# Kernel tuning notes

Hardware: AMD Instinct MI355X
Metric: run time of the kernel (lower is better)

Reference implementation:

```python
import jax, jax.numpy as jnp
import numpy as np

S, B, D = 128, 32, 512
H = 512
L = 2
V = 8000


def _mk_lstm_params(key, in_dim, hid, layers):
    ks = jax.random.split(key, 4 * layers)
    s = 1.0 / np.sqrt(hid)
    W_ih = jnp.stack([jax.random.uniform(ks[4 * j + 0], (4 * hid, in_dim if j == 0 else hid), minval=-s, maxval=s) for j in range(layers)])
    W_hh = jnp.stack([jax.random.uniform(ks[4 * j + 1], (4 * hid, hid), minval=-s, maxval=s) for j in range(layers)])
    b_ih = jnp.stack([jax.random.uniform(ks[4 * j + 2], (4 * hid,), minval=-s, maxval=s) for j in range(layers)])
    b_hh = jnp.stack([jax.random.uniform(ks[4 * j + 3], (4 * hid,), minval=-s, maxval=s) for j in range(layers)])
    return W_ih, W_hh, b_ih, b_hh


def setup_inputs() -> dict:
    key = jax.random.key(0)
    kx, kf, kb, kwf, kwb = jax.random.split(key, 5)
    x = jax.random.normal(kx, (S, B, D), dtype=jnp.float32)
    Wf_ih, Wf_hh, bf_ih, bf_hh = _mk_lstm_params(kf, D, H, L)
    Wb_ih, Wb_hh, bb_ih, bb_hh = _mk_lstm_params(kb, D, H, L)
    s = 1.0 / np.sqrt(H)
    W_fwd = jax.random.uniform(kwf, (V, H), minval=-s, maxval=s)
    b_fwd = jnp.zeros((V,), jnp.float32)
    W_bwd = jax.random.uniform(kwb, (V, H), minval=-s, maxval=s)
    b_bwd = jnp.zeros((V,), jnp.float32)
    return {"x": x,
            "Wf_ih": Wf_ih, "Wf_hh": Wf_hh, "bf_ih": bf_ih, "bf_hh": bf_hh,
            "Wb_ih": Wb_ih, "Wb_hh": Wb_hh, "bb_ih": bb_ih, "bb_hh": bb_hh,
            "W_fwd": W_fwd, "b_fwd": b_fwd, "W_bwd": W_bwd, "b_bwd": b_bwd}


def _stacked_lstm(x_seq, W_ih, W_hh, b_ih, b_hh):
    """x_seq: [S,B,D]; params stacked over layers [L,4H,*]. Returns top-layer h over time: [S,B,H]."""
    layers = W_ih.shape[0]
    batch = x_seq.shape[1]
    h0 = jnp.zeros((layers, batch, H), x_seq.dtype)
    c0 = jnp.zeros((layers, batch, H), x_seq.dtype)

    def step(carry, x_t):
        h, c = carry
        hs, cs = [], []
        inp = x_t
        for j in range(layers):
            gates = inp @ W_ih[j].T + b_ih[j] + h[j] @ W_hh[j].T + b_hh[j]  # [B,4H]
            i_g, f_g, g_g, o_g = jnp.split(gates, 4, axis=-1)
            c_j = jax.nn.sigmoid(f_g) * c[j] + jax.nn.sigmoid(i_g) * jnp.tanh(g_g)
            h_j = jax.nn.sigmoid(o_g) * jnp.tanh(c_j)
            hs.append(h_j)
            cs.append(c_j)
            inp = h_j
        return (jnp.stack(hs), jnp.stack(cs)), inp

    _, out = jax.lax.scan(step, (h0, c0), x_seq)
    return out  # [S,B,H]


def reference(x, Wf_ih, Wf_hh, bf_ih, bf_hh, Wb_ih, Wb_hh, bb_ih, bb_hh, W_fwd, b_fwd, W_bwd, b_bwd):
    fwd_h = _stacked_lstm(x, Wf_ih, Wf_hh, bf_ih, bf_hh)                    # [S,B,H]
    bwd_h = _stacked_lstm(x[::-1], Wb_ih, Wb_hh, bb_ih, bb_hh)[::-1]        # [S,B,H]
    forward_dis = fwd_h @ W_fwd.T + b_fwd                                   # [S,B,V]
    backward_dis = bwd_h @ W_bwd.T + b_bwd                                  # [S,B,V]
    return (forward_dis, backward_dis)
```

## Files before the change

kernel.cpp:

```cpp
#include <hip/hip_runtime.h>

#define SS 128
#define BB 32
#define HH 512
#define VV 8000
#define VPAD 8064

typedef __bf16 bf16_t;
typedef __bf16 bf16x8 __attribute__((ext_vector_type(8)));
typedef float  floatx4 __attribute__((ext_vector_type(4)));
typedef unsigned int u32x4 __attribute__((ext_vector_type(4)));

__device__ __forceinline__ float sigmoidf_(float x) { return 1.0f / (1.0f + expf(-x)); }
__device__ __forceinline__ bf16x8 as_bf16x8(u32x4 v) { return __builtin_bit_cast(bf16x8, v); }

#define WS_FLG   0
#define WS_HHI   1024
#define WS_HLO   (WS_HHI + 524288)
#define WS_XHI   (WS_HLO + 524288)
#define WS_XLO   (WS_XHI + 4194304)
#define WS_HOUT  (WS_XLO + 4194304)
#define WS_WP    (WS_HOUT + 8388608)
#define MEMSET_BYTES WS_XHI

#define SMEM_BYTES 149632


__global__ __launch_bounds__(256)
void prep_x(const float* __restrict__ x, bf16_t* __restrict__ xh, bf16_t* __restrict__ xl) {
    int i = blockIdx.x * 256 + threadIdx.x;
    float v = x[i];
    bf16_t h = (bf16_t)v;
    xh[i] = h;
    xl[i] = (bf16_t)(v - (float)h);
}

__global__ __launch_bounds__(256)
void prep_wp(const float* __restrict__ Wf, const float* __restrict__ Wb, bf16_t* __restrict__ Wp) {
    int i = blockIdx.x * 256 + threadIdx.x;
    int k   = i & 511;
    int rd  = i >> 9;
    int row = rd % 8064;
    int d   = rd / 8064;
    const float* W = d ? Wb : Wf;
    Wp[i] = (row < VV) ? (bf16_t)W[(size_t)row * 512 + k] : (bf16_t)0.0f;
}


__global__ __launch_bounds__(512, 2)
void lstm_persist(const float* __restrict__ Wf_ih, const float* __restrict__ Wf_hh,
                  const float* __restrict__ Wb_ih, const float* __restrict__ Wb_hh,
                  const float* __restrict__ bf_ih, const float* __restrict__ bf_hh,
                  const float* __restrict__ bb_ih, const float* __restrict__ bb_hh,
                  const bf16_t* __restrict__ x_hi, const bf16_t* __restrict__ x_lo,
                  bf16_t* __restrict__ h_hi, bf16_t* __restrict__ h_lo,
                  bf16_t* __restrict__ hout, int* __restrict__ flg)
{
    extern __shared__ char smem[];
    bf16_t* wlds = (bf16_t*)smem;
    float*  pbuf = (float*)(smem + 131072);
    float*  bsum = (float*)(smem + 131072 + 18432);

    const int bid  = blockIdx.x;
    const int d    = bid >> 7;
    const int l    = (bid >> 6) & 1;
    const int s    = bid & 63;
    const int gid  = d * 2 + l;
    const int tid  = threadIdx.x;
    const int lane = tid & 63;
    const int kq   = tid >> 6;
    const int half = kq >> 2;
    const int kb   = kq & 3;
    const int lrow = lane & 15;
    const int quad = lane >> 4;

    const float* Wih = (d ? Wb_ih : Wf_ih) + (size_t)l * (2048 * 512);
    const float* Whh = (d ? Wb_hh : Wf_hh) + (size_t)l * (2048 * 512);

    if (tid < 32) {
        int g = tid >> 3, c = tid & 7;
        int grow = g * 512 + s * 8 + c;
        bsum[tid] = (d ? bb_ih : bf_ih)[l * 2048 + grow] + (d ? bb_hh : bf_hh)[l * 2048 + grow];
    }

    {
        const float* Wsrc = half ? Whh : Wih;
        bf16x8* w8 = (bf16x8*)wlds;
#pragma unroll
        for (int j = 0; j < 4; ++j)
#pragma unroll
            for (int nt = 0; nt < 2; ++nt) {
                int n    = nt * 16 + lrow;
                int grow = (n >> 3) * 512 + s * 8 + (n & 7);
                const float* src = Wsrc + (size_t)grow * 512 + (kb * 128 + j * 32 + quad * 8);
                bf16x8 vh, vl;
#pragma unroll
                for (int e = 0; e < 8; ++e) {
                    float v = src[e];
                    bf16_t hb = (bf16_t)v;
                    vh[e] = hb;
                    vl[e] = (bf16_t)(v - (float)hb);
                }
                int cidx = ((kq * 4 + j) * 2 + nt) * 2;
                w8[(size_t)cidx * 64 + lane]       = vh;
                w8[(size_t)(cidx + 1) * 64 + lane] = vl;
            }
    }
    __syncthreads();

    const bf16x8* wv8 = (const bf16x8*)wlds + (size_t)kq * 1024 + lane;
    const int aoff = lrow * 512 + kb * 128 + quad * 8;
    const bool xwave = (half == 0) && (l == 0);

    float creg = 0.0f;

#pragma unroll 1
    for (int t = 0; t < SS; ++t) {
        const int slot_c = t & 3, slot_p = (t + 3) & 3;

        u32x4 rA0[4], rA1[4], rB0[4], rB1[4];

        if (xwave) {
            int t_x = d ? (SS - 1 - t) : t;
            const bf16_t* ah = x_hi + (size_t)t_x * 16384 + aoff;
            const bf16_t* al = x_lo + (size_t)t_x * 16384 + aoff;
#pragma unroll
            for (int j = 0; j < 4; ++j) {
                rA0[j] = *(const u32x4*)(ah + j * 32);
                rA1[j] = *(const u32x4*)(ah + 8192 + j * 32);
                rB0[j] = *(const u32x4*)(al + j * 32);
                rB1[j] = *(const u32x4*)(al + 8192 + j * 32);
            }
        }

        if (tid < 64) {
            const int *fA, *fB; int tA, tB;
            if (l == 0) { fA = flg + gid * 64;       tA = t;
                          fB = flg + (gid + 1) * 64; tB = t - 3; }
            else        { fA = flg + (gid - 1) * 64; tA = t + 1;
                          fB = flg + gid * 64;       tB = t; }
            for (;;) {
                int a = __hip_atomic_load(fA + tid, __ATOMIC_RELAXED, __HIP_MEMORY_SCOPE_AGENT);
                int b = __hip_atomic_load(fB + tid, __ATOMIC_RELAXED, __HIP_MEMORY_SCOPE_AGENT);
                if (__all((a >= tA) && (b >= tB))) break;
                __builtin_amdgcn_s_sleep(2);
            }
        }
        __syncthreads();

        if (!xwave) {
            const bf16_t *pH, *pL;
            if (half == 0) {
                pH = h_hi + (size_t)((d * 2) * 4 + slot_c) * 16384;
                pL = h_lo + (size_t)((d * 2) * 4 + slot_c) * 16384;
            } else {
                pH = h_hi + (size_t)(gid * 4 + slot_p) * 16384;
                pL = h_lo + (size_t)(gid * 4 + slot_p) * 16384;
            }
            const bf16_t* ah  = pH + aoff;
            const bf16_t* ah2 = ah + 8192;
            const bf16_t* al  = pL + aoff;
            const bf16_t* al2 = al + 8192;
            asm volatile(
                "global_load_dwordx4 %0, %16, off sc1\n\t"
                "global_load_dwordx4 %1, %16, off offset:64 sc1\n\t"
                "global_load_dwordx4 %2, %16, off offset:128 sc1\n\t"
                "global_load_dwordx4 %3, %16, off offset:192 sc1\n\t"
                "global_load_dwordx4 %4, %17, off sc1\n\t"
                "global_load_dwordx4 %5, %17, off offset:64 sc1\n\t"
                "global_load_dwordx4 %6, %17, off offset:128 sc1\n\t"
                "global_load_dwordx4 %7, %17, off offset:192 sc1\n\t"
                "global_load_dwordx4 %8, %18, off sc1\n\t"
                "global_load_dwordx4 %9, %18, off offset:64 sc1\n\t"
                "global_load_dwordx4 %10, %18, off offset:128 sc1\n\t"
                "global_load_dwordx4 %11, %18, off offset:192 sc1\n\t"
                "global_load_dwordx4 %12, %19, off sc1\n\t"
                "global_load_dwordx4 %13, %19, off offset:64 sc1\n\t"
                "global_load_dwordx4 %14, %19, off offset:128 sc1\n\t"
                "global_load_dwordx4 %15, %19, off offset:192 sc1\n\t"
                "s_waitcnt vmcnt(0)"
                : "=&v"(rA0[0]), "=&v"(rA0[1]), "=&v"(rA0[2]), "=&v"(rA0[3]),
                  "=&v"(rA1[0]), "=&v"(rA1[1]), "=&v"(rA1[2]), "=&v"(rA1[3]),
                  "=&v"(rB0[0]), "=&v"(rB0[1]), "=&v"(rB0[2]), "=&v"(rB0[3]),
                  "=&v"(rB1[0]), "=&v"(rB1[1]), "=&v"(rB1[2]), "=&v"(rB1[3])
                : "v"(ah), "v"(ah2), "v"(al), "v"(al2)
                : "memory");
        }

        floatx4 acc00 = {0,0,0,0}, acc01 = {0,0,0,0}, acc10 = {0,0,0,0}, acc11 = {0,0,0,0};
#pragma unroll
        for (int j = 0; j < 4; ++j) {
            bf16x8 b0h = wv8[j * 256];
            bf16x8 b0l = wv8[j * 256 + 64];
            bf16x8 b1h = wv8[j * 256 + 128];
            bf16x8 b1l = wv8[j * 256 + 192];
            bf16x8 ah0 = as_bf16x8(rA0[j]);
            bf16x8 ah1 = as_bf16x8(rA1[j]);
            bf16x8 al0 = as_bf16x8(rB0[j]);
            bf16x8 al1 = as_bf16x8(rB1[j]);
            acc00 = __builtin_amdgcn_mfma_f32_16x16x32_bf16(ah0, b0h, acc00, 0, 0, 0);
            acc00 = __builtin_amdgcn_mfma_f32_16x16x32_bf16(ah0, b0l, acc00, 0, 0, 0);
            acc00 = __builtin_amdgcn_mfma_f32_16x16x32_bf16(al0, b0h, acc00, 0, 0, 0);
            acc01 = __builtin_amdgcn_mfma_f32_16x16x32_bf16(ah0, b1h, acc01, 0, 0, 0);
            acc01 = __builtin_amdgcn_mfma_f32_16x16x32_bf16(ah0, b1l, acc01, 0, 0, 0);
            acc01 = __builtin_amdgcn_mfma_f32_16x16x32_bf16(al0, b1h, acc01, 0, 0, 0);
            acc10 = __builtin_amdgcn_mfma_f32_16x16x32_bf16(ah1, b0h, acc10, 0, 0, 0);
            acc10 = __builtin_amdgcn_mfma_f32_16x16x32_bf16(ah1, b0l, acc10, 0, 0, 0);
            acc10 = __builtin_amdgcn_mfma_f32_16x16x32_bf16(al1, b0h, acc10, 0, 0, 0);
            acc11 = __builtin_amdgcn_mfma_f32_16x16x32_bf16(ah1, b1h, acc11, 0, 0, 0);
            acc11 = __builtin_amdgcn_mfma_f32_16x16x32_bf16(ah1, b1l, acc11, 0, 0, 0);
            acc11 = __builtin_amdgcn_mfma_f32_16x16x32_bf16(al1, b1h, acc11, 0, 0, 0);
        }

        if (half == 0) {
#pragma unroll
            for (int rg = 0; rg < 4; ++rg) {
                pbuf[kb * 1152 + (quad * 4 + rg) * 36 + lrow]           = acc00[rg];
                pbuf[kb * 1152 + (quad * 4 + rg) * 36 + 16 + lrow]      = acc01[rg];
                pbuf[kb * 1152 + (16 + quad * 4 + rg) * 36 + lrow]      = acc10[rg];
                pbuf[kb * 1152 + (16 + quad * 4 + rg) * 36 + 16 + lrow] = acc11[rg];
            }
        }
        __syncthreads();
        if (half == 1) {
#pragma unroll
            for (int rg = 0; rg < 4; ++rg) {
                pbuf[kb * 1152 + (quad * 4 + rg) * 36 + lrow]           += acc00[rg];
                pbuf[kb * 1152 + (quad * 4 + rg) * 36 + 16 + lrow]      += acc01[rg];
                pbuf[kb * 1152 + (16 + quad * 4 + rg) * 36 + lrow]      += acc10[rg];
                pbuf[kb * 1152 + (16 + quad * 4 + rg) * 36 + 16 + lrow] += acc11[rg];
            }
        }
        __syncthreads();

        if (tid < 256) {
            int b = tid >> 3, c = tid & 7;
            float gi = 0.f, gf = 0.f, gg = 0.f, go = 0.f;
#pragma unroll
            for (int kbb = 0; kbb < 4; ++kbb) {
                int base = kbb * 1152 + b * 36 + c;
                gi += pbuf[base];
                gf += pbuf[base + 8];
                gg += pbuf[base + 16];
                go += pbuf[base + 24];
            }
            gi += bsum[c]; gf += bsum[8 + c]; gg += bsum[16 + c]; go += bsum[24 + c];
            float cn = sigmoidf_(gf) * creg + sigmoidf_(gi) * tanhf(gg);
            float hn = sigmoidf_(go) * tanhf(cn);
            creg = cn;
            bf16_t hh = (bf16_t)hn;
            bf16_t hl = (bf16_t)(hn - (float)hh);
            int col = s * 8 + c;
            size_t ho = (size_t)(gid * 4 + slot_c) * 16384 + (size_t)b * HH + col;
            unsigned int vh = (unsigned int)__builtin_bit_cast(unsigned short, hh);
            unsigned int vl = (unsigned int)__builtin_bit_cast(unsigned short, hl);
            const bf16_t* ph = h_hi + ho;
            const bf16_t* pl = h_lo + ho;
            asm volatile(
                "global_store_short %0, %2, off sc1\n\t"
                "global_store_short %1, %3, off sc1\n\t"
                "s_waitcnt vmcnt(0)"
                :: "v"(ph), "v"(pl), "v"(vh), "v"(vl)
                : "memory");
            if (l == 1) {
                int t_x = d ? (SS - 1 - t) : t;
                hout[((size_t)(d * SS + t_x) * BB + b) * HH + col] = hh;
            }
        }

        __syncthreads();
        if (tid == 0) {
            __hip_atomic_store(flg + gid * 64 + s, t + 1,
                               __ATOMIC_RELAXED, __HIP_MEMORY_SCOPE_AGENT);
        }
    }
}

__global__ __launch_bounds__(256)
void proj_gemm(const bf16_t* __restrict__ hA, const bf16_t* __restrict__ Wp,
               const float* __restrict__ b_fwd, const float* __restrict__ b_bwd,
               float* __restrict__ out)
{
    const int bid = blockIdx.x;
    const int nb  = (bid & 7) + ((bid >> 8) << 3);
    const int mb  = (bid >> 3) & 31;
    if (nb >= 63) return;
    const int d  = blockIdx.z;
    const int n0 = nb * 128;
    const int m0 = mb * 128;
    const bf16_t* A  = hA + (size_t)d * (SS * BB * HH);
    const bf16_t* Bw = Wp + (size_t)d * ((size_t)VPAD * HH);
    const float* bias = d ? b_bwd : b_fwd;
    float* O = out + (size_t)d * ((size_t)SS * BB * VV);

    __shared__ __align__(16) bf16_t lds_a[128 * 40];
    __shared__ __align__(16) bf16_t lds_b[128 * 40];

    const int tid  = threadIdx.x;
    const int lane = tid & 63;
    const int wv   = tid >> 6;
    const int wm   = wv >> 1, wn = wv & 1;
    const int lrow = lane & 15, quad = lane >> 4;

    floatx4 acc[4][4];
#pragma unroll
    for (int i = 0; i < 4; ++i)
#pragma unroll
        for (int j = 0; j < 4; ++j) acc[i][j] = (floatx4){0.f, 0.f, 0.f, 0.f};

    for (int k0 = 0; k0 < HH; k0 += 32) {
        __syncthreads();
#pragma unroll
        for (int q2 = 0; q2 < 2; ++q2) {
            int q = tid * 2 + q2;
            int row = q >> 2, cc = (q & 3) * 8;
            *(bf16x8*)(&lds_a[row * 40 + cc]) = *(const bf16x8*)(A  + (size_t)(m0 + row) * HH + k0 + cc);
            *(bf16x8*)(&lds_b[row * 40 + cc]) = *(const bf16x8*)(Bw + (size_t)(n0 + row) * HH + k0 + cc);
        }
        __syncthreads();
        bf16x8 af[4], bf4[4];
#pragma unroll
        for (int i = 0; i < 4; ++i) {
            af[i]  = *(const bf16x8*)(&lds_a[(wm * 64 + i * 16 + lrow) * 40 + quad * 8]);
            bf4[i] = *(const bf16x8*)(&lds_b[(wn * 64 + i * 16 + lrow) * 40 + quad * 8]);
        }
#pragma unroll
        for (int i = 0; i < 4; ++i)
#pragma unroll
            for (int j = 0; j < 4; ++j)
                acc[i][j] = __builtin_amdgcn_mfma_f32_16x16x32_bf16(af[i], bf4[j], acc[i][j], 0, 0, 0);
    }

#pragma unroll
    for (int j = 0; j < 4; ++j) {
        int n = n0 + wn * 64 + j * 16 + lrow;
        if (n < VV) {
            float bv = bias[n];
#pragma unroll
            for (int i = 0; i < 4; ++i) {
                int mbase = m0 + wm * 64 + i * 16 + quad * 4;
#pragma unroll
                for (int rg = 0; rg < 4; ++rg)
                    O[(size_t)(mbase + rg) * VV + n] = acc[i][j][rg] + bv;
            }
        }
    }
}


extern "C" void kernel_launch(void* const* d_in, const int* in_sizes, int n_in,
                              void* d_out, int out_size, void* d_ws, size_t ws_size,
                              hipStream_t stream)
{
    const float* x     = (const float*)d_in[0];
    const float* Wf_ih = (const float*)d_in[1];
    const float* Wf_hh = (const float*)d_in[2];
    const float* bf_ih = (const float*)d_in[3];
    const float* bf_hh = (const float*)d_in[4];
    const float* Wb_ih = (const float*)d_in[5];
    const float* Wb_hh = (const float*)d_in[6];
    const float* bb_ih = (const float*)d_in[7];
    const float* bb_hh = (const float*)d_in[8];
    const float* W_fwd = (const float*)d_in[9];
    const float* b_fwd = (const float*)d_in[10];
    const float* W_bwd = (const float*)d_in[11];
    const float* b_bwd = (const float*)d_in[12];
    float* out = (float*)d_out;
    (void)in_sizes; (void)n_in; (void)out_size; (void)ws_size;

    char* ws = (char*)d_ws;
    int*    flg  = (int*)   (ws + WS_FLG);
    bf16_t* h_hi = (bf16_t*)(ws + WS_HHI);
    bf16_t* h_lo = (bf16_t*)(ws + WS_HLO);
    bf16_t* x_hi = (bf16_t*)(ws + WS_XHI);
    bf16_t* x_lo = (bf16_t*)(ws + WS_XLO);
    bf16_t* hout = (bf16_t*)(ws + WS_HOUT);
    bf16_t* Wp   = (bf16_t*)(ws + WS_WP);

    (void)hipFuncSetAttribute(reinterpret_cast<const void*>(lstm_persist),
                              hipFuncAttributeMaxDynamicSharedMemorySize, SMEM_BYTES);

    hipMemsetAsync(ws, 0, MEMSET_BYTES, stream);

    prep_x <<<dim3(8192),  256, 0, stream>>>(x, x_hi, x_lo);
    prep_wp<<<dim3(32256), 256, 0, stream>>>(W_fwd, W_bwd, Wp);

    lstm_persist<<<dim3(256), dim3(512), SMEM_BYTES, stream>>>(
        Wf_ih, Wf_hh, Wb_ih, Wb_hh, bf_ih, bf_hh, bb_ih, bb_hh,
        x_hi, x_lo, h_hi, h_lo, hout, flg);

    proj_gemm<<<dim3(2048, 1, 2), 256, 0, stream>>>(hout, Wp, b_fwd, b_bwd, out);
}
```

Baseline: 1.550 ms.

## Cut per-step recurrence latency with LDS atomics, split waits, and deferred hout store

The two-phase partial-sum reduction, which needed an extra barrier, becomes LDS atomicAdd into a pre-zeroed buffer that the gate threads clear after reading. The h loads are interleaved and waited on in two halves, so the MFMAs on the first K-chunks can start before all loads finish. The flag-polling wave moves to the last wave and drops its sleep. The top-layer hout store now happens after the flag is published, taking it off the critical path. The risks are LDS atomic contention, and spin polling without sleep adding memory traffic.

```diff
diff --git a/kernel.cpp b/kernel.cpp
--- a/kernel.cpp
+++ b/kernel.cpp
@@ -83,6 +83,8 @@
         bsum[tid] = (d ? bb_ih : bf_ih)[l * 2048 + grow] + (d ? bb_hh : bf_hh)[l * 2048 + grow];
     }
 
+    for (int i = tid; i < 4608; i += 512) pbuf[i] = 0.0f;
+
     {
         const float* Wsrc = half ? Whh : Wih;
         bf16x8* w8 = (bf16x8*)wlds;
@@ -133,17 +135,17 @@
             }
         }
 
-        if (tid < 64) {
+        if (tid >= 448) {
+            const int ln = tid & 63;
             const int *fA, *fB; int tA, tB;
             if (l == 0) { fA = flg + gid * 64;       tA = t;
                           fB = flg + (gid + 1) * 64; tB = t - 3; }
             else        { fA = flg + (gid - 1) * 64; tA = t + 1;
                           fB = flg + gid * 64;       tB = t; }
             for (;;) {
-                int a = __hip_atomic_load(fA + tid, __ATOMIC_RELAXED, __HIP_MEMORY_SCOPE_AGENT);
-                int b = __hip_atomic_load(fB + tid, __ATOMIC_RELAXED, __HIP_MEMORY_SCOPE_AGENT);
+                int a = __hip_atomic_load(fA + ln, __ATOMIC_RELAXED, __HIP_MEMORY_SCOPE_AGENT);
+                int b = __hip_atomic_load(fB + ln, __ATOMIC_RELAXED, __HIP_MEMORY_SCOPE_AGENT);
                 if (__all((a >= tA) && (b >= tB))) break;
-                __builtin_amdgcn_s_sleep(2);
             }
         }
         __syncthreads();
@@ -163,22 +165,22 @@
             const bf16_t* al2 = al + 8192;
             asm volatile(
                 "global_load_dwordx4 %0, %16, off sc1\n\t"
+                "global_load_dwordx4 %4, %17, off sc1\n\t"
+                "global_load_dwordx4 %8, %18, off sc1\n\t"
+                "global_load_dwordx4 %12, %19, off sc1\n\t"
                 "global_load_dwordx4 %1, %16, off offset:64 sc1\n\t"
+                "global_load_dwordx4 %5, %17, off offset:64 sc1\n\t"
+                "global_load_dwordx4 %9, %18, off offset:64 sc1\n\t"
+                "global_load_dwordx4 %13, %19, off offset:64 sc1\n\t"
                 "global_load_dwordx4 %2, %16, off offset:128 sc1\n\t"
+                "global_load_dwordx4 %6, %17, off offset:128 sc1\n\t"
+                "global_load_dwordx4 %10, %18, off offset:128 sc1\n\t"
+                "global_load_dwordx4 %14, %19, off offset:128 sc1\n\t"
                 "global_load_dwordx4 %3, %16, off offset:192 sc1\n\t"
-                "global_load_dwordx4 %4, %17, off sc1\n\t"
-                "global_load_dwordx4 %5, %17, off offset:64 sc1\n\t"
-                "global_load_dwordx4 %6, %17, off offset:128 sc1\n\t"
                 "global_load_dwordx4 %7, %17, off offset:192 sc1\n\t"
-                "global_load_dwordx4 %8, %18, off sc1\n\t"
-                "global_load_dwordx4 %9, %18, off offset:64 sc1\n\t"
-                "global_load_dwordx4 %10, %18, off offset:128 sc1\n\t"
                 "global_load_dwordx4 %11, %18, off offset:192 sc1\n\t"
-                "global_load_dwordx4 %12, %19, off sc1\n\t"
-                "global_load_dwordx4 %13, %19, off offset:64 sc1\n\t"
-                "global_load_dwordx4 %14, %19, off offset:128 sc1\n\t"
                 "global_load_dwordx4 %15, %19, off offset:192 sc1\n\t"
-                "s_waitcnt vmcnt(0)"
+                "s_waitcnt vmcnt(8)"
                 : "=&v"(rA0[0]), "=&v"(rA0[1]), "=&v"(rA0[2]), "=&v"(rA0[3]),
                   "=&v"(rA1[0]), "=&v"(rA1[1]), "=&v"(rA1[2]), "=&v"(rA1[3]),
                   "=&v"(rB0[0]), "=&v"(rB0[1]), "=&v"(rB0[2]), "=&v"(rB0[3]),
@@ -190,6 +192,11 @@
         floatx4 acc00 = {0,0,0,0}, acc01 = {0,0,0,0}, acc10 = {0,0,0,0}, acc11 = {0,0,0,0};
 #pragma unroll
         for (int j = 0; j < 4; ++j) {
+            if (j == 2 && !xwave) {
+                asm volatile("s_waitcnt vmcnt(0)"
+                             : "+v"(rA0[2]), "+v"(rA0[3]), "+v"(rA1[2]), "+v"(rA1[3]),
+                               "+v"(rB0[2]), "+v"(rB0[3]), "+v"(rB1[2]), "+v"(rB1[3]));
+            }
             bf16x8 b0h = wv8[j * 256];
             bf16x8 b0l = wv8[j * 256 + 64];
             bf16x8 b1h = wv8[j * 256 + 128];
@@ -212,27 +219,19 @@
             acc11 = __builtin_amdgcn_mfma_f32_16x16x32_bf16(al1, b1h, acc11, 0, 0, 0);
         }
 
-        if (half == 0) {
+        {
+            float* pb = pbuf + kb * 1152;
 #pragma unroll
             for (int rg = 0; rg < 4; ++rg) {
-                pbuf[kb * 1152 + (quad * 4 + rg) * 36 + lrow]           = acc00[rg];
-                pbuf[kb * 1152 + (quad * 4 + rg) * 36 + 16 + lrow]      = acc01[rg];
-                pbuf[kb * 1152 + (16 + quad * 4 + rg) * 36 + lrow]      = acc10[rg];
-                pbuf[kb * 1152 + (16 + quad * 4 + rg) * 36 + 16 + lrow] = acc11[rg];
-            }
-        }
-        __syncthreads();
-        if (half == 1) {
-#pragma unroll
-            for (int rg = 0; rg < 4; ++rg) {
-                pbuf[kb * 1152 + (quad * 4 + rg) * 36 + lrow]           += acc00[rg];
-                pbuf[kb * 1152 + (quad * 4 + rg) * 36 + 16 + lrow]      += acc01[rg];
-                pbuf[kb * 1152 + (16 + quad * 4 + rg) * 36 + lrow]      += acc10[rg];
-                pbuf[kb * 1152 + (16 + quad * 4 + rg) * 36 + 16 + lrow] += acc11[rg];
-            }
-        }
-        __syncthreads();
-
+                atomicAdd(pb + (quad * 4 + rg) * 36 + lrow,           acc00[rg]);
+                atomicAdd(pb + (quad * 4 + rg) * 36 + 16 + lrow,      acc01[rg]);
+                atomicAdd(pb + (16 + quad * 4 + rg) * 36 + lrow,      acc10[rg]);
+                atomicAdd(pb + (16 + quad * 4 + rg) * 36 + 16 + lrow, acc11[rg]);
+            }
+        }
+        __syncthreads();
+
+        bf16_t hh_keep = (bf16_t)0.0f;
         if (tid < 256) {
             int b = tid >> 3, c = tid & 7;
             float gi = 0.f, gf = 0.f, gg = 0.f, go = 0.f;
@@ -243,6 +242,10 @@
                 gf += pbuf[base + 8];
                 gg += pbuf[base + 16];
                 go += pbuf[base + 24];
+                pbuf[base]      = 0.f;
+                pbuf[base + 8]  = 0.f;
+                pbuf[base + 16] = 0.f;
+                pbuf[base + 24] = 0.f;
             }
             gi += bsum[c]; gf += bsum[8 + c]; gg += bsum[16 + c]; go += bsum[24 + c];
             float cn = sigmoidf_(gf) * creg + sigmoidf_(gi) * tanhf(gg);
@@ -250,6 +253,7 @@
             creg = cn;
             bf16_t hh = (bf16_t)hn;
             bf16_t hl = (bf16_t)(hn - (float)hh);
+            hh_keep = hh;
             int col = s * 8 + c;
             size_t ho = (size_t)(gid * 4 + slot_c) * 16384 + (size_t)b * HH + col;
             unsigned int vh = (unsigned int)__builtin_bit_cast(unsigned short, hh);
@@ -262,16 +266,18 @@
                 "s_waitcnt vmcnt(0)"
                 :: "v"(ph), "v"(pl), "v"(vh), "v"(vl)
                 : "memory");
-            if (l == 1) {
-                int t_x = d ? (SS - 1 - t) : t;
-                hout[((size_t)(d * SS + t_x) * BB + b) * HH + col] = hh;
-            }
         }
 
         __syncthreads();
         if (tid == 0) {
             __hip_atomic_store(flg + gid * 64 + s, t + 1,
                                __ATOMIC_RELAXED, __HIP_MEMORY_SCOPE_AGENT);
+        }
+        if (l == 1 && tid < 256) {
+            int b = tid >> 3, c = tid & 7;
+            int col = s * 8 + c;
+            int t_x = d ? (SS - 1 - t) : t;
+            hout[((size_t)(d * SS + t_x) * BB + b) * HH + col] = hh_keep;
         }
     }
 }
```

After: 2.508 ms. 1.62x slower.

## Split inter-block flag waits per wave and overlap h loads with MFMA

Applied to the files above, without the earlier changes.

Replaces the single pre-step spin by wave 0 plus block barrier with per-wave spins: each wave waits only on the flag it depends on. The layer-0 wait on layer-1 progress (the WAR hazard on the ring slot) moves to just before the h store. The h loads are reordered so the first half of MFMAs can start after a partial vmcnt wait. The hout store is moved after the flag publish, taking it off the critical path. This shortens the per-timestep serialized latency chain, at the cost of more polling traffic and subtler memory-ordering correctness.

```diff
diff --git a/kernel.cpp b/kernel.cpp
--- a/kernel.cpp
+++ b/kernel.cpp
@@ -112,6 +112,11 @@
     const int aoff = lrow * 512 + kb * 128 + quad * 8;
     const bool xwave = (half == 0) && (l == 0);
 
+    const int* wflag = nullptr;
+    int  woff = 0;
+    if (half == 1)      { wflag = flg + gid * 64;       woff = 0; }
+    else if (l == 1)    { wflag = flg + (gid - 1) * 64; woff = 1; }
+
     float creg = 0.0f;
 
 #pragma unroll 1
@@ -119,6 +124,15 @@
         const int slot_c = t & 3, slot_p = (t + 3) & 3;
 
         u32x4 rA0[4], rA1[4], rB0[4], rB1[4];
+
+        if (wflag) {
+            const int thr = t + woff;
+            for (;;) {
+                int v = __hip_atomic_load(wflag + lane, __ATOMIC_RELAXED, __HIP_MEMORY_SCOPE_AGENT);
+                if (__all(v >= thr)) break;
+                __builtin_amdgcn_s_sleep(2);
+            }
+        }
 
         if (xwave) {
             int t_x = d ? (SS - 1 - t) : t;
@@ -131,24 +145,7 @@
                 rB0[j] = *(const u32x4*)(al + j * 32);
                 rB1[j] = *(const u32x4*)(al + 8192 + j * 32);
             }
-        }
-
-        if (tid < 64) {
-            const int *fA, *fB; int tA, tB;
-            if (l == 0) { fA = flg + gid * 64;       tA = t;
-                          fB = flg + (gid + 1) * 64; tB = t - 3; }
-            else        { fA = flg + (gid - 1) * 64; tA = t + 1;
-                          fB = flg + gid * 64;       tB = t; }
-            for (;;) {
-                int a = __hip_atomic_load(fA + tid, __ATOMIC_RELAXED, __HIP_MEMORY_SCOPE_AGENT);
-                int b = __hip_atomic_load(fB + tid, __ATOMIC_RELAXED, __HIP_MEMORY_SCOPE_AGENT);
-                if (__all((a >= tA) && (b >= tB))) break;
-                __builtin_amdgcn_s_sleep(2);
-            }
-        }
-        __syncthreads();
-
-        if (!xwave) {
+        } else {
             const bf16_t *pH, *pL;
             if (half == 0) {
                 pH = h_hi + (size_t)((d * 2) * 4 + slot_c) * 16384;
@@ -163,22 +160,22 @@
             const bf16_t* al2 = al + 8192;
             asm volatile(
                 "global_load_dwordx4 %0, %16, off sc1\n\t"
+                "global_load_dwordx4 %4, %17, off sc1\n\t"
+                "global_load_dwordx4 %8, %18, off sc1\n\t"
+                "global_load_dwordx4 %12, %19, off sc1\n\t"
                 "global_load_dwordx4 %1, %16, off offset:64 sc1\n\t"
+                "global_load_dwordx4 %5, %17, off offset:64 sc1\n\t"
+                "global_load_dwordx4 %9, %18, off offset:64 sc1\n\t"
+                "global_load_dwordx4 %13, %19, off offset:64 sc1\n\t"
                 "global_load_dwordx4 %2, %16, off offset:128 sc1\n\t"
+                "global_load_dwordx4 %6, %17, off offset:128 sc1\n\t"
+                "global_load_dwordx4 %10, %18, off offset:128 sc1\n\t"
+                "global_load_dwordx4 %14, %19, off offset:128 sc1\n\t"
                 "global_load_dwordx4 %3, %16, off offset:192 sc1\n\t"
-                "global_load_dwordx4 %4, %17, off sc1\n\t"
-                "global_load_dwordx4 %5, %17, off offset:64 sc1\n\t"
-                "global_load_dwordx4 %6, %17, off offset:128 sc1\n\t"
                 "global_load_dwordx4 %7, %17, off offset:192 sc1\n\t"
-                "global_load_dwordx4 %8, %18, off sc1\n\t"
-                "global_load_dwordx4 %9, %18, off offset:64 sc1\n\t"
-                "global_load_dwordx4 %10, %18, off offset:128 sc1\n\t"
-                "global_load_dwordx4 %11, %18, off offset:192 sc1\n\t"
-                "global_load_dwordx4 %12, %19, off sc1\n\t"
-                "global_load_dwordx4 %13, %19, off offset:64 sc1\n\t"
-                "global_load_dwordx4 %14, %19, off offset:128 sc1\n\t"
+                "global_load_dwordx4 %11, %19, off offset:192 sc1\n\t"
                 "global_load_dwordx4 %15, %19, off offset:192 sc1\n\t"
-                "s_waitcnt vmcnt(0)"
+                "s_waitcnt vmcnt(8)"
                 : "=&v"(rA0[0]), "=&v"(rA0[1]), "=&v"(rA0[2]), "=&v"(rA0[3]),
                   "=&v"(rA1[0]), "=&v"(rA1[1]), "=&v"(rA1[2]), "=&v"(rA1[3]),
                   "=&v"(rB0[0]), "=&v"(rB0[1]), "=&v"(rB0[2]), "=&v"(rB0[3]),
@@ -190,6 +187,11 @@
         floatx4 acc00 = {0,0,0,0}, acc01 = {0,0,0,0}, acc10 = {0,0,0,0}, acc11 = {0,0,0,0};
 #pragma unroll
         for (int j = 0; j < 4; ++j) {
+            if (j == 2 && !xwave) {
+                asm volatile("s_waitcnt vmcnt(0)"
+                             : "+v"(rA0[2]), "+v"(rA0[3]), "+v"(rA1[2]), "+v"(rA1[3]),
+                               "+v"(rB0[2]), "+v"(rB0[3]), "+v"(rB1[2]), "+v"(rB1[3]));
+            }
             bf16x8 b0h = wv8[j * 256];
             bf16x8 b0l = wv8[j * 256 + 64];
             bf16x8 b1h = wv8[j * 256 + 128];
@@ -233,23 +235,34 @@
         }
         __syncthreads();
 
+        bf16_t hh_keep = (bf16_t)0.0f;
         if (tid < 256) {
+            if (l == 0 && t >= 4) {
+                const int* gf = flg + (gid + 1) * 64;
+                const int thr = t - 3;
+                for (;;) {
+                    int v = __hip_atomic_load(gf + lane, __ATOMIC_RELAXED, __HIP_MEMORY_SCOPE_AGENT);
+                    if (__all(v >= thr)) break;
+                    __builtin_amdgcn_s_sleep(2);
+                }
+            }
             int b = tid >> 3, c = tid & 7;
-            float gi = 0.f, gf = 0.f, gg = 0.f, go = 0.f;
+            float gi = 0.f, gf_ = 0.f, gg = 0.f, go = 0.f;
 #pragma unroll
             for (int kbb = 0; kbb < 4; ++kbb) {
                 int base = kbb * 1152 + b * 36 + c;
-                gi += pbuf[base];
-                gf += pbuf[base + 8];
-                gg += pbuf[base + 16];
-                go += pbuf[base + 24];
-            }
-            gi += bsum[c]; gf += bsum[8 + c]; gg += bsum[16 + c]; go += bsum[24 + c];
-            float cn = sigmoidf_(gf) * creg + sigmoidf_(gi) * tanhf(gg);
+                gi  += pbuf[base];
+                gf_ += pbuf[base + 8];
+                gg  += pbuf[base + 16];
+                go  += pbuf[base + 24];
+            }
+            gi += bsum[c]; gf_ += bsum[8 + c]; gg += bsum[16 + c]; go += bsum[24 + c];
+            float cn = sigmoidf_(gf_) * creg + sigmoidf_(gi) * tanhf(gg);
             float hn = sigmoidf_(go) * tanhf(cn);
             creg = cn;
             bf16_t hh = (bf16_t)hn;
             bf16_t hl = (bf16_t)(hn - (float)hh);
+            hh_keep = hh;
             int col = s * 8 + c;
             size_t ho = (size_t)(gid * 4 + slot_c) * 16384 + (size_t)b * HH + col;
             unsigned int vh = (unsigned int)__builtin_bit_cast(unsigned short, hh);
@@ -262,16 +275,18 @@
                 "s_waitcnt vmcnt(0)"
                 :: "v"(ph), "v"(pl), "v"(vh), "v"(vl)
                 : "memory");
-            if (l == 1) {
-                int t_x = d ? (SS - 1 - t) : t;
-                hout[((size_t)(d * SS + t_x) * BB + b) * HH + col] = hh;
-            }
         }
 
         __syncthreads();
         if (tid == 0) {
             __hip_atomic_store(flg + gid * 64 + s, t + 1,
                                __ATOMIC_RELAXED, __HIP_MEMORY_SCOPE_AGENT);
+        }
+        if (l == 1 && tid < 256) {
+            int b = tid >> 3, c = tid & 7;
+            int col = s * 8 + c;
+            int t_x = d ? (SS - 1 - t) : t;
+            hout[((size_t)(d * SS + t_x) * BB + b) * HH + col] = hh_keep;
         }
     }
 }
```

Result: faster. 1.501 ms (-3.1%).
